# Optimization experiments

Hardware: AMD Instinct MI355X
Metric: run time of the kernel (lower is better)

## Reference

```python
import jax, jax.numpy as jnp
import numpy as np

C = 256
EPS = 1e-5


def setup_inputs() -> dict:
    key = jax.random.key(0)
    ks = jax.random.split(key, 11)
    B, L = 4, 4096
    s = 1.0 / np.sqrt(C)
    inp = {
        'x': jax.random.normal(ks[0], (B, C, L), dtype=jnp.float32),
        'gamma': jnp.ones((C,), jnp.float32),
        'beta': jnp.zeros((C,), jnp.float32),
        'wq': jax.random.normal(ks[1], (C, C), jnp.float32) * s,
        'bq': jax.random.normal(ks[2], (C,), jnp.float32) * 0.01,
        'wk': jax.random.normal(ks[3], (C, C), jnp.float32) * s,
        'bk': jax.random.normal(ks[4], (C,), jnp.float32) * 0.01,
        'wv': jax.random.normal(ks[5], (C, C), jnp.float32) * s,
        'bv': jax.random.normal(ks[6], (C,), jnp.float32) * 0.01,
        'wp': jax.random.normal(ks[7], (C, C), jnp.float32) * s,
        'bp': jax.random.normal(ks[8], (C,), jnp.float32) * 0.01,
    }
    return inp


def reference(x, gamma, beta, wq, bq, wk, bk, wv, bv, wp, bp):
    # BatchNorm1d (training mode): normalize over batch and length dims
    mean = jnp.mean(x, axis=(0, 2), keepdims=True)          # [1,C,1]
    var = jnp.var(x, axis=(0, 2), keepdims=True)            # biased var, as torch BN
    h = (x - mean) * jax.lax.rsqrt(var + EPS)
    h = h * gamma[None, :, None] + beta[None, :, None]

    # 1x1 convs == channel-mixing matmuls: [C_out,C_in] x [B,C_in,L]
    q = jnp.einsum('oc,bcl->bol', wq, h) + bq[None, :, None]
    k = jnp.einsum('oc,bcl->bol', wk, h) + bk[None, :, None]
    v = jnp.einsum('oc,bcl->bol', wv, h) + bv[None, :, None]

    c = q.shape[1]
    scale = jnp.asarray(int(c) ** (-0.5), q.dtype)
    # w[b,i,j] = sum_c q[b,c,i] k[b,c,j]
    w = jnp.einsum('bci,bcj->bij', q, k) * scale
    w = jax.nn.softmax(w, axis=2)
    # torch: h[b,c,i] = sum_j v[b,c,j] * w[b,i,j]
    h = jnp.einsum('bcj,bij->bci', v, w)

    h = jnp.einsum('oc,bcl->bol', wp, h) + bp[None, :, None]
    return x + h
```

## Files before the change

### kernel.cpp

```cpp
#include <hip/hip_runtime.h>
#include <math.h>

typedef unsigned short u16;
typedef unsigned int u32;
typedef short s16x8 __attribute__((ext_vector_type(8)));
typedef float f32x4 __attribute__((ext_vector_type(4)));
typedef float f32x16 __attribute__((ext_vector_type(16)));

static constexpr int Cc = 256;
static constexpr int Ll = 4096;
static constexpr int Bb = 4;

__device__ __forceinline__ u16 f2b(float f) {
    union { float f; unsigned u; } v; v.f = f;
    unsigned r = v.u + 0x7FFF + ((v.u >> 16) & 1);
    return (u16)(r >> 16);
}
__device__ __forceinline__ float b2f(u16 h) {
    union { unsigned u; float f; } v; v.u = ((unsigned)h) << 16; return v.f;
}

__device__ __forceinline__ void gload_lds16(const u16* g, u16* l) {
    __builtin_amdgcn_global_load_lds(
        (const __attribute__((address_space(1))) u32*)g,
        (__attribute__((address_space(3))) u32*)l, 16, 0, 0);
}

__device__ __forceinline__ u32 cvtpk(float lo, float hi) {
    u32 r;
    asm volatile("v_cvt_pk_bf16_f32 %0, %1, %2" : "=v"(r) : "v"(lo), "v"(hi));
    return r;
}

__global__ void k_transpose(const float* __restrict__ x, u16* __restrict__ XT,
                            float* __restrict__ sums) {
    int lt = blockIdx.x, ct = blockIdx.y, b = blockIdx.z, t = threadIdx.x;
    int l0 = lt * 64, c0 = ct * 64;
    __shared__ u16 tile[64][65];
    __shared__ float red[2][4][64];
    int ll = t & 63, cb = t >> 6;
    #pragma unroll
    for (int rep = 0; rep < 16; rep++) {
        int cl = cb * 16 + rep;
        tile[cl][ll] = f2b(x[(size_t)(b * Cc + c0 + cl) * Ll + l0 + ll]);
    }
    __syncthreads();
    int cl2 = t & 63, lb = t >> 6;
    float s = 0.f, s2 = 0.f;
    #pragma unroll
    for (int rep = 0; rep < 16; rep++) {
        int ll2 = lb * 16 + rep;
        u16 hv = tile[cl2][ll2];
        XT[(size_t)(b * Ll + l0 + ll2) * Cc + c0 + cl2] = hv;
        float v = b2f(hv);
        s += v; s2 += v * v;
    }
    red[0][lb][cl2] = s;
    red[1][lb][cl2] = s2;
    __syncthreads();
    if (t < 64) {
        float ss = red[0][0][t] + red[0][1][t] + red[0][2][t] + red[0][3][t];
        float ss2 = red[1][0][t] + red[1][1][t] + red[1][2][t] + red[1][3][t];
        atomicAdd(&sums[c0 + t], ss);
        atomicAdd(&sums[256 + c0 + t], ss2);
    }
}

__global__ void k_fold(const float* __restrict__ wq, const float* __restrict__ bq,
                       const float* __restrict__ wk, const float* __restrict__ bk,
                       const float* __restrict__ wv, const float* __restrict__ bv,
                       const float* __restrict__ wp,
                       const float* __restrict__ gamma, const float* __restrict__ beta,
                       const float* __restrict__ sums,
                       u16* __restrict__ Wqkv, float* __restrict__ biasQKV,
                       u16* __restrict__ Wp16) {
    int m = blockIdx.x, t = threadIdx.x;
    if (m >= 768) {
        int row = m - 768;
        Wp16[row * Cc + t] = f2b(wp[row * Cc + t]);
        return;
    }
    const float inv_n = 1.f / (Bb * Ll);
    float mean = sums[t] * inv_n;
    float var  = sums[256 + t] * inv_n - mean * mean;
    float rstd = rsqrtf(var + 1e-5f);
    float a  = gamma[t] * rstd;
    float cB = beta[t] - mean * a;
    int type = m >> 8, row = m & 255;
    const float* W  = (type == 0) ? wq : (type == 1) ? wk : wv;
    const float* bs = (type == 0) ? bq : (type == 1) ? bk : bv;
    float wval = W[row * Cc + t];
    float s2 = (type == 0) ? 0.09016844005556021f : 1.0f;
    Wqkv[m * Cc + t] = f2b(wval * a * s2);
    __shared__ float rs[256];
    rs[t] = wval * cB;
    __syncthreads();
    for (int off = 128; off > 0; off >>= 1) {
        if (t < off) rs[t] += rs[t + off];
        __syncthreads();
    }
    if (t == 0) biasQKV[m] = (bs[row] + rs[0]) * s2;
}

__launch_bounds__(256, 2)
__global__ void k_qkv(const u16* __restrict__ XT, const u16* __restrict__ Wqkv,
                      const float* __restrict__ biasQKV,
                      u16* __restrict__ QT, u16* __restrict__ KT, u16* __restrict__ V) {
    int ly = blockIdx.x, b = blockIdx.y, oh = blockIdx.z;
    int t = threadIdx.x, w = t >> 6, lane = t & 63;
    int l16 = lane & 15, quad = lane >> 4;
    int l0 = ly * 64;
    __shared__ u16 Xs[64][264];
    {
        int row = t >> 2, chunk = t & 3;
        const u16* src = XT + (size_t)(b * Ll + l0 + row) * Cc + chunk * 64;
        u16* dst = &Xs[row][chunk * 64];
        #pragma unroll
        for (int u = 0; u < 8; u++)
            *(uint4*)(dst + u * 8) = *(const uint4*)(src + u * 8);
    }
    __syncthreads();
    for (int ox = oh * 6; ox < oh * 6 + 6; ox++) {
        int o0 = ox * 64;
        s16x8 af[8];
        {
            const u16* wrow = Wqkv + (size_t)(o0 + w * 16 + l16) * Cc + quad * 8;
            #pragma unroll
            for (int ks = 0; ks < 8; ks++) af[ks] = *(const s16x8*)(wrow + ks * 32);
        }
        f32x4 acc[4];
        #pragma unroll
        for (int ns = 0; ns < 4; ns++)
            #pragma unroll
            for (int r = 0; r < 4; r++) acc[ns][r] = 0.f;
        #pragma unroll
        for (int ks = 0; ks < 8; ks++) {
            #pragma unroll
            for (int ns = 0; ns < 4; ns++) {
                s16x8 bf = *(const s16x8*)(&Xs[ns * 16 + l16][ks * 32 + quad * 8]);
                acc[ns] = __builtin_amdgcn_mfma_f32_16x16x32_bf16(af[ks], bf, acc[ns], 0, 0, 0);
            }
        }
        int obase = o0 + w * 16 + quad * 4;
        float bias[4];
        #pragma unroll
        for (int r = 0; r < 4; r++) bias[r] = biasQKV[obase + r];
        #pragma unroll
        for (int ns = 0; ns < 4; ns++) {
            int l = l0 + ns * 16 + l16;
            if (ox < 8) {
                u16* dstbase = (ox < 4) ? QT : KT;
                int oo = obase - ((ox < 4) ? 0 : 256);
                ushort4 pk;
                pk.x = f2b(acc[ns][0] + bias[0]);
                pk.y = f2b(acc[ns][1] + bias[1]);
                pk.z = f2b(acc[ns][2] + bias[2]);
                pk.w = f2b(acc[ns][3] + bias[3]);
                *(ushort4*)(dstbase + (size_t)(b * Ll + l) * Cc + oo) = pk;
            } else {
                #pragma unroll
                for (int r = 0; r < 4; r++) {
                    int o = obase + r - 512;
                    V[(size_t)(b * Cc + o) * Ll + l] = f2b(acc[ns][r] + bias[r]);
                }
            }
        }
    }
}

__launch_bounds__(512, 2)
__global__ void k_attn(const u16* __restrict__ QT, const u16* __restrict__ KT,
                       const u16* __restrict__ V, u16* __restrict__ Opart,
                       float* __restrict__ Lpart) {
    int id = blockIdx.x;
    int xcd = id & 7, local = id >> 3;
    int b = xcd >> 1;
    int u = local * 2 + (xcd & 1);
    int itile = u >> 1;
    int jh = u & 1;
    int t = threadIdx.x, w = t >> 6, lane = t & 63;
    int iw = w & 3, jsub = w >> 2;
    int l31 = lane & 31, hi = lane >> 5;

    __shared__ u16 lds_buf[65536];
    __shared__ float Lred[2][4][32];

    s16x8 qf[16];
    {
        const u16* qbase = QT + (size_t)(b * Ll + itile * 128 + iw * 32 + l31) * Cc + hi * 8;
        #pragma unroll
        for (int ks = 0; ks < 16; ks++) qf[ks] = *(const s16x8*)(qbase + ks * 16);
    }

    const u16* kcur = KT + (size_t)(b * Ll + jh * 2048 + l31) * Cc + hi * 8;
    const u16* vcur = V + (size_t)(b * Cc + l31) * Ll + jh * 2048 + hi * 8;
    int kwo = w * 16;
    size_t vwo = (size_t)((w >> 2) * 32) * Ll + (w & 3) * 16;
    int ldw = w * 512;

#define STAGE_K(c) { u16* kd = lds_buf + (c) * 16384 + ldw;  \
    gload_lds16(kcur + kwo,        kd);          \
    gload_lds16(kcur + kwo + 128,  kd + 4096);   \
    gload_lds16(kcur + kwo + 8192, kd + 8192);   \
    gload_lds16(kcur + kwo + 8320, kd + 12288);  \
    kcur += 64 * Cc; }
#define STAGE_V(c) { u16* vd = lds_buf + 32768 + (c) * 16384 + ldw;  \
    gload_lds16(vcur + vwo,          vd);          \
    gload_lds16(vcur + vwo + 262144, vd + 4096);   \
    gload_lds16(vcur + vwo + 524288, vd + 8192);   \
    gload_lds16(vcur + vwo + 786432, vd + 12288);  \
    vcur += 64; }

    STAGE_K(0); STAGE_V(0); STAGE_K(1); STAGE_V(1);

    f32x16 of[8];
    #pragma unroll
    for (int ct = 0; ct < 8; ct++)
        #pragma unroll
        for (int r = 0; r < 16; r++) of[ct][r] = 0.f;
    float lsum = 0.f;

    asm volatile("s_waitcnt vmcnt(12)" ::: "memory");
    __builtin_amdgcn_s_barrier();

    int aoff = jsub * 8192 + lane * 8;
    int boff = jsub * 1024 + lane * 8;

    for (int it = 0; it < 32; it++) {
        const u16* KaC = lds_buf + (it & 1) * 16384;
        const u16* VbC = lds_buf + 32768 + (it & 1) * 16384;

        f32x16 s0, s1;
        #pragma unroll
        for (int r = 0; r < 16; r++) { s0[r] = 0.f; s1[r] = 0.f; }
        __builtin_amdgcn_s_setprio(1);
        #pragma unroll
        for (int ks = 0; ks < 16; ks += 2) {
            s16x8 kf0 = *(const s16x8*)(KaC + aoff + ks * 512);
            s16x8 kf1 = *(const s16x8*)(KaC + aoff + ks * 512 + 512);
            s0 = __builtin_amdgcn_mfma_f32_32x32x16_bf16(kf0, qf[ks], s0, 0, 0, 0);
            s1 = __builtin_amdgcn_mfma_f32_32x32x16_bf16(kf1, qf[ks + 1], s1, 0, 0, 0);
        }
        __builtin_amdgcn_s_setprio(0);

        float p[16];
        #pragma unroll
        for (int r = 0; r < 16; r++) {
            p[r] = __builtin_amdgcn_exp2f(s0[r] + s1[r]);
            lsum += p[r];
        }
        u32 paw[2][4];
        #pragma unroll
        for (int js = 0; js < 2; js++) {
            int o = js * 8;
            u32 a0 = cvtpk(p[o + 0], p[o + 1]);
            u32 b0 = cvtpk(p[o + 4], p[o + 5]);
            u32 a1 = cvtpk(p[o + 2], p[o + 3]);
            u32 b1 = cvtpk(p[o + 6], p[o + 7]);
            asm volatile("v_permlane32_swap_b32 %0, %1" : "+v"(a0), "+v"(b0));
            asm volatile("v_permlane32_swap_b32 %0, %1" : "+v"(a1), "+v"(b1));
            paw[js][0] = a0; paw[js][1] = a1; paw[js][2] = b0; paw[js][3] = b1;
        }

        asm volatile("s_waitcnt lgkmcnt(0)" ::: "memory");
        if (it < 31) asm volatile("s_waitcnt vmcnt(8)" ::: "memory");
        else         asm volatile("s_waitcnt vmcnt(0)" ::: "memory");
        __builtin_amdgcn_s_barrier();
        if (it < 30) STAGE_K(it & 1);

        __builtin_amdgcn_s_setprio(1);
        #pragma unroll
        for (int js = 0; js < 2; js++) {
            union { u32 u[4]; s16x8 v; } pa;
            pa.u[0] = paw[js][0]; pa.u[1] = paw[js][1];
            pa.u[2] = paw[js][2]; pa.u[3] = paw[js][3];
            #pragma unroll
            for (int ct = 0; ct < 8; ct++) {
                s16x8 bf = *(const s16x8*)(VbC + ct * 2048 + boff + js * 512);
                of[ct] = __builtin_amdgcn_mfma_f32_32x32x16_bf16(pa.v, bf, of[ct], 0, 0, 0);
            }
        }
        __builtin_amdgcn_s_setprio(0);

        if (it < 31) {
            asm volatile("s_waitcnt lgkmcnt(0)" ::: "memory");
            if (it < 30) asm volatile("s_waitcnt vmcnt(8)" ::: "memory");
            else         asm volatile("s_waitcnt vmcnt(4)" ::: "memory");
            __builtin_amdgcn_s_barrier();
            if (it < 30) STAGE_V(it & 1);
        }
    }
#undef STAGE_K
#undef STAGE_V

    lsum += __shfl_xor(lsum, 32);
    if (lane < 32) Lred[jsub][iw][l31] = lsum;
    __syncthreads();
    int mi0 = (jh * 4 + b) * Ll + itile * 128;
    if (jsub == 0 && lane < 32)
        Lpart[mi0 + iw * 32 + l31] = Lred[0][iw][l31] + Lred[1][iw][l31];

    float* Om = (float*)lds_buf;
    if (jsub == 1) {
        #pragma unroll
        for (int ct = 0; ct < 8; ct++)
            #pragma unroll
            for (int r = 0; r < 16; r++)
                Om[((iw * 8 + ct) * 16 + r) * 64 + lane] = of[ct][r];
    }
    __syncthreads();
    if (jsub == 0) {
        #pragma unroll
        for (int ct = 0; ct < 8; ct++)
            #pragma unroll
            for (int r = 0; r < 16; r++) {
                float val = of[ct][r] + Om[((iw * 8 + ct) * 16 + r) * 64 + lane];
                int rl = (r & 3) + 8 * (r >> 2) + 4 * hi;
                Opart[(size_t)(mi0 + iw * 32 + rl) * 256 + ct * 32 + l31] = f2b(val);
            }
    }
}

__global__ void k_merge(const u16* __restrict__ Opart, const float* __restrict__ Lpart,
                        u16* __restrict__ OT) {
    int id = blockIdx.x, t = threadIdx.x;
    int b = id >> 6, itile = id & 63;
    int row = t >> 2, seg = t & 3;
    size_t i0 = ((size_t)(0 + b) * 64 + itile) * 64 + row;
    size_t i1 = ((size_t)(4 + b) * 64 + itile) * 64 + row;
    float inv = 1.f / (Lpart[i0] + Lpart[i1]);
    const u16* p0 = Opart + i0 * 256 + seg * 64;
    const u16* p1 = Opart + i1 * 256 + seg * 64;
    u16* dst = OT + (size_t)(b * Ll + itile * 64 + row) * Cc + seg * 64;
    #pragma unroll
    for (int k = 0; k < 8; k++) {
        ushort4 a0 = *(const ushort4*)(p0 + k * 8 + 0);
        ushort4 b0 = *(const ushort4*)(p0 + k * 8 + 4);
        ushort4 a1 = *(const ushort4*)(p1 + k * 8 + 0);
        ushort4 b1 = *(const ushort4*)(p1 + k * 8 + 4);
        ushort4 oA, oB;
        oA.x = f2b((b2f(a0.x) + b2f(a1.x)) * inv);
        oA.y = f2b((b2f(a0.y) + b2f(a1.y)) * inv);
        oA.z = f2b((b2f(a0.z) + b2f(a1.z)) * inv);
        oA.w = f2b((b2f(a0.w) + b2f(a1.w)) * inv);
        oB.x = f2b((b2f(b0.x) + b2f(b1.x)) * inv);
        oB.y = f2b((b2f(b0.y) + b2f(b1.y)) * inv);
        oB.z = f2b((b2f(b0.z) + b2f(b1.z)) * inv);
        oB.w = f2b((b2f(b0.w) + b2f(b1.w)) * inv);
        *(ushort4*)(dst + k * 8 + 0) = oA;
        *(ushort4*)(dst + k * 8 + 4) = oB;
    }
}

__launch_bounds__(256, 2)
__global__ void k_proj(const u16* __restrict__ OT, const u16* __restrict__ Opart,
                       const float* __restrict__ Lpart, int fused,
                       const u16* __restrict__ Wp16,
                       const float* __restrict__ bp, const float* __restrict__ x,
                       float* __restrict__ out) {
    int ly = blockIdx.x, b = blockIdx.y, oh = blockIdx.z;
    int t = threadIdx.x, w = t >> 6, lane = t & 63;
    int l16 = lane & 15, quad = lane >> 4;
    int l0 = ly * 64;
    __shared__ u16 Os[64][264];
    {
        int row = t >> 2, chunk = t & 3;
        u16* dst = &Os[row][chunk * 64];
        if (fused) {
            size_t i0 = ((size_t)(0 + b) * Ll + l0 + row);
            size_t i1 = ((size_t)(4 + b) * Ll + l0 + row);
            float inv = 1.f / (Lpart[i0] + Lpart[i1]);
            const u16* p0 = Opart + i0 * 256 + chunk * 64;
            const u16* p1 = Opart + i1 * 256 + chunk * 64;
            #pragma unroll
            for (int k = 0; k < 8; k++) {
                ushort4 a0 = *(const ushort4*)(p0 + k * 8 + 0);
                ushort4 b0 = *(const ushort4*)(p0 + k * 8 + 4);
                ushort4 a1 = *(const ushort4*)(p1 + k * 8 + 0);
                ushort4 b1 = *(const ushort4*)(p1 + k * 8 + 4);
                ushort4 oA, oB;
                oA.x = f2b((b2f(a0.x) + b2f(a1.x)) * inv);
                oA.y = f2b((b2f(a0.y) + b2f(a1.y)) * inv);
                oA.z = f2b((b2f(a0.z) + b2f(a1.z)) * inv);
                oA.w = f2b((b2f(a0.w) + b2f(a1.w)) * inv);
                oB.x = f2b((b2f(b0.x) + b2f(b1.x)) * inv);
                oB.y = f2b((b2f(b0.y) + b2f(b1.y)) * inv);
                oB.z = f2b((b2f(b0.z) + b2f(b1.z)) * inv);
                oB.w = f2b((b2f(b0.w) + b2f(b1.w)) * inv);
                *(ushort4*)(dst + k * 8 + 0) = oA;
                *(ushort4*)(dst + k * 8 + 4) = oB;
            }
        } else {
            const u16* src = OT + (size_t)(b * Ll + l0 + row) * Cc + chunk * 64;
            #pragma unroll
            for (int u = 0; u < 8; u++)
                *(uint4*)(dst + u * 8) = *(const uint4*)(src + u * 8);
        }
    }
    __syncthreads();
    for (int ox = oh * 2; ox < oh * 2 + 2; ox++) {
        int o0 = ox * 64;
        s16x8 af[8];
        {
            const u16* wrow = Wp16 + (size_t)(o0 + w * 16 + l16) * Cc + quad * 8;
            #pragma unroll
            for (int ks = 0; ks < 8; ks++) af[ks] = *(const s16x8*)(wrow + ks * 32);
        }
        f32x4 acc[4];
        #pragma unroll
        for (int ns = 0; ns < 4; ns++)
            #pragma unroll
            for (int r = 0; r < 4; r++) acc[ns][r] = 0.f;
        #pragma unroll
        for (int ks = 0; ks < 8; ks++) {
            #pragma unroll
            for (int ns = 0; ns < 4; ns++) {
                s16x8 bf = *(const s16x8*)(&Os[ns * 16 + l16][ks * 32 + quad * 8]);
                acc[ns] = __builtin_amdgcn_mfma_f32_16x16x32_bf16(af[ks], bf, acc[ns], 0, 0, 0);
            }
        }
        int ob = o0 + w * 16 + quad * 4;
        float bias[4];
        #pragma unroll
        for (int r = 0; r < 4; r++) bias[r] = bp[ob + r];
        #pragma unroll
        for (int ns = 0; ns < 4; ns++) {
            #pragma unroll
            for (int r = 0; r < 4; r++) {
                int o = ob + r;
                int l = l0 + ns * 16 + l16;
                size_t idx = (size_t)(b * Cc + o) * Ll + l;
                out[idx] = x[idx] + bias[r] + acc[ns][r];
            }
        }
    }
}

extern "C" void kernel_launch(void* const* d_in, const int* in_sizes, int n_in,
                              void* d_out, int out_size, void* d_ws, size_t ws_size,
                              hipStream_t stream) {
    const float* x     = (const float*)d_in[0];
    const float* gamma = (const float*)d_in[1];
    const float* beta  = (const float*)d_in[2];
    const float* wq    = (const float*)d_in[3];
    const float* bq    = (const float*)d_in[4];
    const float* wk    = (const float*)d_in[5];
    const float* bk    = (const float*)d_in[6];
    const float* wv    = (const float*)d_in[7];
    const float* bv    = (const float*)d_in[8];
    const float* wp    = (const float*)d_in[9];
    const float* bp    = (const float*)d_in[10];
    float* out = (float*)d_out;
    char* ws = (char*)d_ws;

    float* sums    = (float*)(ws + 0);
    float* biasQKV = (float*)(ws + 2048);
    u16*   Wqkv    = (u16*)(ws + 8192);
    u16*   Wp16    = (u16*)(ws + 401408);
    u16*   XT      = (u16*)(ws + 532480);
    u16*   QT      = (u16*)(ws + 8921088);
    u16*   KT      = (u16*)(ws + 17309696);
    u16*   V       = (u16*)(ws + 25698304);
    u16*   OT      = XT;

    const size_t opart_off = 34086912;
    const size_t lpart_off = opart_off + 16777216;
    const size_t needed    = lpart_off + 131072;
    int fused = (ws_size >= needed) ? 1 : 0;
    u16*   Opart = fused ? (u16*)(ws + opart_off) : (u16*)d_out;
    float* Lpart = (float*)(ws + (fused ? lpart_off : opart_off));

    (void)hipMemsetAsync(sums, 0, 2048, stream);
    k_transpose<<<dim3(64, 4, 4), 256, 0, stream>>>(x, XT, sums);
    k_fold<<<1024, 256, 0, stream>>>(wq, bq, wk, bk, wv, bv, wp, gamma, beta,
                                     sums, Wqkv, biasQKV, Wp16);
    k_qkv<<<dim3(64, 4, 2), 256, 0, stream>>>(XT, Wqkv, biasQKV, QT, KT, V);
    k_attn<<<256, 512, 0, stream>>>(QT, KT, V, Opart, Lpart);
    if (!fused)
        k_merge<<<256, 256, 0, stream>>>(Opart, Lpart, OT);
    k_proj<<<dim3(64, 4, 2), 256, 0, stream>>>(OT, Opart, Lpart, fused,
                                               Wp16, bp, x, out);
}
```

Measured before the change: 229.9 us.

## Load K fragments directly from global into registers instead of LDS staging

Drops the double-buffered LDS staging of K tiles in the attention loop. Each wave now loads its 16 K fragments straight from global memory into registers at the top of every iteration, and V takes over the freed LDS space. This removes one barrier and the K DMA bookkeeping per iteration. In exchange, K reads repeat across the waves that share a j sub-tile, global latency sits right before the QK MFMAs with no prefetch, and the compiler's wait on those loads may also stall on the in-flight V prefetches.

```diff
diff --git a/kernel.cpp b/kernel.cpp
--- a/kernel.cpp
+++ b/kernel.cpp
@@ -192,26 +192,20 @@
         for (int ks = 0; ks < 16; ks++) qf[ks] = *(const s16x8*)(qbase + ks * 16);
     }
 
-    const u16* kcur = KT + (size_t)(b * Ll + jh * 2048 + l31) * Cc + hi * 8;
+    const u16* kcur = KT + (size_t)(b * Ll + jh * 2048 + jsub * 32 + l31) * Cc + hi * 8;
+
     const u16* vcur = V + (size_t)(b * Cc + l31) * Ll + jh * 2048 + hi * 8;
-    int kwo = w * 16;
     size_t vwo = (size_t)((w >> 2) * 32) * Ll + (w & 3) * 16;
     int ldw = w * 512;
 
-#define STAGE_K(c) { u16* kd = lds_buf + (c) * 16384 + ldw;  \
-    gload_lds16(kcur + kwo,        kd);          \
-    gload_lds16(kcur + kwo + 128,  kd + 4096);   \
-    gload_lds16(kcur + kwo + 8192, kd + 8192);   \
-    gload_lds16(kcur + kwo + 8320, kd + 12288);  \
-    kcur += 64 * Cc; }
-#define STAGE_V(c) { u16* vd = lds_buf + 32768 + (c) * 16384 + ldw;  \
+#define STAGE_V(c) { u16* vd = lds_buf + (c) * 16384 + ldw;  \
     gload_lds16(vcur + vwo,          vd);          \
     gload_lds16(vcur + vwo + 262144, vd + 4096);   \
     gload_lds16(vcur + vwo + 524288, vd + 8192);   \
     gload_lds16(vcur + vwo + 786432, vd + 12288);  \
     vcur += 64; }
 
-    STAGE_K(0); STAGE_V(0); STAGE_K(1); STAGE_V(1);
+    STAGE_V(0); STAGE_V(1);
 
     f32x16 of[8];
     #pragma unroll
@@ -220,15 +214,15 @@
         for (int r = 0; r < 16; r++) of[ct][r] = 0.f;
     float lsum = 0.f;
 
-    asm volatile("s_waitcnt vmcnt(12)" ::: "memory");
-    __builtin_amdgcn_s_barrier();
-
-    int aoff = jsub * 8192 + lane * 8;
     int boff = jsub * 1024 + lane * 8;
 
     for (int it = 0; it < 32; it++) {
-        const u16* KaC = lds_buf + (it & 1) * 16384;
-        const u16* VbC = lds_buf + 32768 + (it & 1) * 16384;
+        const u16* VbC = lds_buf + (it & 1) * 16384;
+
+        s16x8 kf[16];
+        #pragma unroll
+        for (int ks = 0; ks < 16; ks++) kf[ks] = *(const s16x8*)(kcur + ks * 16);
+        kcur += 64 * Cc;
 
         f32x16 s0, s1;
         #pragma unroll
@@ -236,10 +230,8 @@
         __builtin_amdgcn_s_setprio(1);
         #pragma unroll
         for (int ks = 0; ks < 16; ks += 2) {
-            s16x8 kf0 = *(const s16x8*)(KaC + aoff + ks * 512);
-            s16x8 kf1 = *(const s16x8*)(KaC + aoff + ks * 512 + 512);
-            s0 = __builtin_amdgcn_mfma_f32_32x32x16_bf16(kf0, qf[ks], s0, 0, 0, 0);
-            s1 = __builtin_amdgcn_mfma_f32_32x32x16_bf16(kf1, qf[ks + 1], s1, 0, 0, 0);
+            s0 = __builtin_amdgcn_mfma_f32_32x32x16_bf16(kf[ks], qf[ks], s0, 0, 0, 0);
+            s1 = __builtin_amdgcn_mfma_f32_32x32x16_bf16(kf[ks + 1], qf[ks + 1], s1, 0, 0, 0);
         }
         __builtin_amdgcn_s_setprio(0);
 
@@ -262,11 +254,7 @@
             paw[js][0] = a0; paw[js][1] = a1; paw[js][2] = b0; paw[js][3] = b1;
         }
 
-        asm volatile("s_waitcnt lgkmcnt(0)" ::: "memory");
-        if (it < 31) asm volatile("s_waitcnt vmcnt(8)" ::: "memory");
-        else         asm volatile("s_waitcnt vmcnt(0)" ::: "memory");
-        __builtin_amdgcn_s_barrier();
-        if (it < 30) STAGE_K(it & 1);
+        if (it == 0) __builtin_amdgcn_s_barrier();
 
         __builtin_amdgcn_s_setprio(1);
         #pragma unroll
@@ -284,13 +272,10 @@
 
         if (it < 31) {
             asm volatile("s_waitcnt lgkmcnt(0)" ::: "memory");
-            if (it < 30) asm volatile("s_waitcnt vmcnt(8)" ::: "memory");
-            else         asm volatile("s_waitcnt vmcnt(4)" ::: "memory");
             __builtin_amdgcn_s_barrier();
             if (it < 30) STAGE_V(it & 1);
         }
     }
-#undef STAGE_K
 #undef STAGE_V
 
     lsum += __shfl_xor(lsum, 32);
```

Result: slower. 378.9 us (+64.8%).
